# Kernel optimization log

Hardware: AMD Instinct MI355X
Metric: run time of the kernel (lower is better)

## Reference

```python
import jax, jax.numpy as jnp
import numpy as np

B, S, D, H = 4, 2048, 512, 8
DEPTH = D // H
EPS = 1e-6

def setup_inputs() -> dict:
    key = jax.random.key(0)
    ks = jax.random.split(key, 5)
    scale = 1.0 / np.sqrt(D)
    return {
        "x": jax.random.normal(ks[0], (B, S, D), dtype=jnp.float32),
        "wq": jax.random.normal(ks[1], (D, D), dtype=jnp.float32) * scale,
        "wk": jax.random.normal(ks[2], (D, D), dtype=jnp.float32) * scale,
        "wv": jax.random.normal(ks[3], (D, D), dtype=jnp.float32) * scale,
        "wo": jax.random.normal(ks[4], (D, D), dtype=jnp.float32) * scale,
        "bo": jnp.zeros((D,), dtype=jnp.float32),
        "gamma": jnp.ones((D,), dtype=jnp.float32),
        "beta": jnp.zeros((D,), dtype=jnp.float32),
    }

def _split_heads(t):
    # [B,S,D] -> [B,H,S,depth]
    return t.reshape(B, S, H, DEPTH).transpose(0, 2, 1, 3)

def reference(x, wq, wk, wv, wo, bo, gamma, beta):
    q = _split_heads(x @ wq)
    k = _split_heads(x @ wk)
    v = _split_heads(x @ wv)
    logits = jnp.einsum("bhqd,bhkd->bhqk", q, k) / jnp.sqrt(jnp.float32(DEPTH))
    attn = jax.nn.softmax(logits, axis=-1)  # dropout is identity at inference
    ctx = jnp.einsum("bhqk,bhkd->bhqd", attn, v)
    ctx = ctx.transpose(0, 2, 1, 3).reshape(B, S, D)
    out = ctx @ wo + bo
    resid = x + out  # output dropout identity at inference
    mu = jnp.mean(resid, axis=-1, keepdims=True)
    var = jnp.mean(jnp.square(resid - mu), axis=-1, keepdims=True)
    return (resid - mu) / jnp.sqrt(var + EPS) * gamma + beta
```

## Files before the change

kernel.cpp:

```cpp
#include <hip/hip_runtime.h>
#include <hip/hip_bf16.h>

typedef __attribute__((ext_vector_type(8))) short short8;
typedef __attribute__((ext_vector_type(4))) float f32x4;

constexpr int B_ = 4, S_ = 2048, D_ = 512, H_ = 8, DP_ = 64;
constexpr int M_ = B_ * S_;

__device__ __forceinline__ unsigned short f2b(float f) {
    __hip_bfloat16 h = __float2bfloat16(f);
    return *reinterpret_cast<unsigned short*>(&h);
}

__device__ __forceinline__ void gload_lds16(const unsigned short* g, unsigned short* l) {
    __builtin_amdgcn_global_load_lds((const __attribute__((address_space(1))) void*)g,
                                     (__attribute__((address_space(3))) void*)l, 16, 0, 0);
}

#define MFMA16(a, b, c) __builtin_amdgcn_mfma_f32_16x16x32_bf16((a), (b), (c), 0, 0, 0)
#define ASM_BAR() asm volatile("s_barrier" ::: "memory")

__global__ __launch_bounds__(256)
void convert_x(const float* __restrict__ in, unsigned short* __restrict__ out) {
    int i = blockIdx.x * 256 + threadIdx.x;
    float4 v = ((const float4*)in)[i];
    ushort4 o;
    o.x = f2b(v.x); o.y = f2b(v.y); o.z = f2b(v.z); o.w = f2b(v.w);
    ((ushort4*)out)[i] = o;
}

__global__ __launch_bounds__(256)
void transpose_w(const float* __restrict__ w0, const float* __restrict__ w1,
                 const float* __restrict__ w2, const float* __restrict__ w3,
                 unsigned short* __restrict__ outw) {
    const float* in = (blockIdx.z == 0) ? w0 : (blockIdx.z == 1) ? w1
                     : (blockIdx.z == 2) ? w2 : w3;
    unsigned short* out = outw + (size_t)blockIdx.z * D_ * D_;
    __shared__ float t[64][65];
    int k0 = blockIdx.x * 64, n0 = blockIdx.y * 64;
    int tx = threadIdx.x & 63, ty = threadIdx.x >> 6;
#pragma unroll
    for (int i = 0; i < 16; i++) {
        int r = ty * 16 + i;
        t[r][tx] = in[(size_t)(k0 + r) * D_ + n0 + tx];
    }
    __syncthreads();
#pragma unroll
    for (int i = 0; i < 16; i++) {
        int r = ty * 16 + i;
        out[(size_t)(n0 + r) * D_ + k0 + tx] = f2b(t[tx][r]);
    }
}

__global__ __launch_bounds__(256, 2)
void gemm_qkv(const unsigned short* __restrict__ X,
              const unsigned short* __restrict__ Wt,
              unsigned short* __restrict__ QKV) {
    const unsigned short* Bt = Wt + (size_t)blockIdx.z * D_ * D_;
    unsigned short* out = QKV + (size_t)blockIdx.z * M_ * D_;
    int m0 = blockIdx.x * 128, n0 = blockIdx.y * 128;
    int tid = threadIdx.x;
    int wave = tid >> 6, lane = tid & 63, l16 = lane & 15, quad = lane >> 4;
    int wm = (wave >> 1) * 64, wn = (wave & 1) * 64;

    __shared__ __align__(16) unsigned short As[128][40];
    __shared__ __align__(16) unsigned short Bs[128][40];

    f32x4 acc[4][4];
    const f32x4 zf = {0.f, 0.f, 0.f, 0.f};
#pragma unroll
    for (int i = 0; i < 4; i++)
#pragma unroll
        for (int j = 0; j < 4; j++) acc[i][j] = zf;

    for (int k0 = 0; k0 < D_; k0 += 32) {
        __syncthreads();
#pragma unroll
        for (int i = 0; i < 2; i++) {
            int c = tid + i * 256;
            int row = c >> 2, off = (c & 3) * 8;
            *(short8*)&As[row][off] = *(const short8*)(X + (size_t)(m0 + row) * D_ + k0 + off);
            *(short8*)&Bs[row][off] = *(const short8*)(Bt + (size_t)(n0 + row) * D_ + k0 + off);
        }
        __syncthreads();
        short8 af[4], bf[4];
#pragma unroll
        for (int mt = 0; mt < 4; mt++) af[mt] = *(const short8*)&As[wm + mt * 16 + l16][quad * 8];
#pragma unroll
        for (int nt = 0; nt < 4; nt++) bf[nt] = *(const short8*)&Bs[wn + nt * 16 + l16][quad * 8];
#pragma unroll
        for (int mt = 0; mt < 4; mt++)
#pragma unroll
            for (int nt = 0; nt < 4; nt++)
                acc[mt][nt] = MFMA16(af[mt], bf[nt], acc[mt][nt]);
    }
#pragma unroll
    for (int mt = 0; mt < 4; mt++)
#pragma unroll
        for (int nt = 0; nt < 4; nt++)
#pragma unroll
            for (int r = 0; r < 4; r++) {
                int m = m0 + wm + mt * 16 + quad * 4 + r;
                int n = n0 + wn + nt * 16 + l16;
                int bb = m >> 11, ss = m & 2047, hh = n >> 6, dd = n & 63;
                out[(((size_t)bb * H_ + hh) * S_ + ss) * DP_ + dd] = f2b(acc[mt][nt][r]);
            }
}

__global__ __launch_bounds__(256, 2)
void gemm_vt(const unsigned short* __restrict__ X,
             const unsigned short* __restrict__ Wt,
             unsigned short* __restrict__ Vt) {
    int bb = blockIdx.z;
    int m0 = blockIdx.x * 128, n0 = blockIdx.y * 128;
    int tid = threadIdx.x;
    int wave = tid >> 6, lane = tid & 63, l16 = lane & 15, quad = lane >> 4;
    int wm = (wave >> 1) * 64, wn = (wave & 1) * 64;

    __shared__ __align__(16) unsigned short As[128][40];
    __shared__ __align__(16) unsigned short Bs[128][40];

    f32x4 acc[4][4];
    const f32x4 zf = {0.f, 0.f, 0.f, 0.f};
#pragma unroll
    for (int i = 0; i < 4; i++)
#pragma unroll
        for (int j = 0; j < 4; j++) acc[i][j] = zf;

    for (int k0 = 0; k0 < D_; k0 += 32) {
        __syncthreads();
#pragma unroll
        for (int i = 0; i < 2; i++) {
            int c = tid + i * 256;
            int row = c >> 2, off = (c & 3) * 8;
            *(short8*)&As[row][off] = *(const short8*)(Wt + (size_t)(m0 + row) * D_ + k0 + off);
            *(short8*)&Bs[row][off] = *(const short8*)(X + (size_t)(bb * S_ + n0 + row) * D_ + k0 + off);
        }
        __syncthreads();
        short8 af[4], bf[4];
#pragma unroll
        for (int mt = 0; mt < 4; mt++) af[mt] = *(const short8*)&As[wm + mt * 16 + l16][quad * 8];
#pragma unroll
        for (int nt = 0; nt < 4; nt++) bf[nt] = *(const short8*)&Bs[wn + nt * 16 + l16][quad * 8];
#pragma unroll
        for (int mt = 0; mt < 4; mt++)
#pragma unroll
            for (int nt = 0; nt < 4; nt++)
                acc[mt][nt] = MFMA16(af[mt], bf[nt], acc[mt][nt]);
    }
#pragma unroll
    for (int mt = 0; mt < 4; mt++)
#pragma unroll
        for (int nt = 0; nt < 4; nt++)
#pragma unroll
            for (int r = 0; r < 4; r++) {
                int m = m0 + wm + mt * 16 + quad * 4 + r;
                int n = n0 + wn + nt * 16 + l16;
                Vt[((size_t)bb * D_ + m) * S_ + n] = f2b(acc[mt][nt][r]);
            }
}

__global__ __launch_bounds__(256, 4)
void flash_attn(const unsigned short* __restrict__ Qg, const unsigned short* __restrict__ Kg,
                const unsigned short* __restrict__ Vt, unsigned short* __restrict__ ctx) {
    int bid0 = blockIdx.x;
    int bid = (bid0 & 7) * 128 + (bid0 >> 3);
    int qt = bid & 31, hh = (bid >> 5) & 7, bb = bid >> 8;
    int tid = threadIdx.x;
    int wave = tid >> 6, lane = tid & 63, l16 = lane & 15, quad = lane >> 4;
    int qh = quad >> 1, ql = quad & 1;

    size_t bh = ((size_t)bb * H_ + hh) * S_ * DP_;
    const unsigned short* Qb = Qg + bh;
    const unsigned short* Kb = Kg + bh;
    const unsigned short* Vb = Vt + bh;

    __shared__ __align__(16) unsigned short Kls[2][64][64];
    __shared__ __align__(16) unsigned short Vls[2][64][64];
    __shared__ __align__(16) unsigned short Ps[4][16][64];

    const int psw = l16 & 7;
    const int drow = (lane >> 3) & 7;
    const int dsw = (lane & 7) ^ drow;

    short8 qf0, qf1;
    {
        const unsigned short* qp = Qb + (size_t)(qt * 64 + wave * 16 + l16) * DP_ + quad * 8;
        qf0 = *(const short8*)qp;
        qf1 = *(const short8*)(qp + 32);
    }

    auto stage = [&](int kv, int b) {
#pragma unroll
        for (int j = 0; j < 2; j++) {
            int r8 = (wave * 2 + j) * 8;
            int r = r8 + drow;
            gload_lds16(Kb + (size_t)(kv + r) * DP_ + dsw * 8, &Kls[b][r8][0]);
            gload_lds16(Vb + (size_t)r * S_ + kv + dsw * 8,    &Vls[b][r8][0]);
        }
    };

    stage(0, 0);
    stage(64, 1);
    asm volatile("s_waitcnt vmcnt(4)" ::: "memory");
    ASM_BAR();

    const f32x4 zf = {0.f, 0.f, 0.f, 0.f};
    f32x4 oacc[4];
#pragma unroll
    for (int i = 0; i < 4; i++) oacc[i] = zf;
    float m2 = -1e30f;
    float lrow = 0.f;
    constexpr float c1 = 0.125f * 1.44269504088896f;

    int cur = 0;
    for (int t = 0; t < 32; t++) {
        __builtin_amdgcn_s_setprio(1);
        f32x4 sacc[4];
#pragma unroll
        for (int nt = 0; nt < 4; nt++) {
            const unsigned short* kr = &Kls[cur][nt * 16 + l16][0];
            short8 kf0 = *(const short8*)(kr + ((quad ^ psw) * 8));
            short8 kf1 = *(const short8*)(kr + (((quad ^ 4) ^ psw) * 8));
            f32x4 s = zf;
            s = MFMA16(kf0, qf0, s);
            s = MFMA16(kf1, qf1, s);
            sacc[nt] = s;
        }
        __builtin_amdgcn_s_setprio(0);

        float t4[4];
#pragma unroll
        for (int nt = 0; nt < 4; nt++)
            t4[nt] = fmaxf(fmaxf(sacc[nt][0], sacc[nt][1]), fmaxf(sacc[nt][2], sacc[nt][3]));
        float g = fmaxf(fmaxf(t4[0], t4[1]), fmaxf(t4[2], t4[3]));
        g = fmaxf(g, __shfl_xor(g, 16));
        g = fmaxf(g, __shfl_xor(g, 32));
        g *= c1;
        float alpha = 1.0f;
        bool need = !__all(g <= m2 + 8.0f);
        if (need) {
            float m2n = fmaxf(m2, g);
            alpha = __builtin_amdgcn_exp2f(m2 - m2n);
            m2 = m2n;
        }
        float rs = 0.f;
#pragma unroll
        for (int nt = 0; nt < 4; nt++) {
            float p0 = __builtin_amdgcn_exp2f(__builtin_fmaf(sacc[nt][0], c1, -m2));
            float p1 = __builtin_amdgcn_exp2f(__builtin_fmaf(sacc[nt][1], c1, -m2));
            float p2 = __builtin_amdgcn_exp2f(__builtin_fmaf(sacc[nt][2], c1, -m2));
            float p3 = __builtin_amdgcn_exp2f(__builtin_fmaf(sacc[nt][3], c1, -m2));
            rs += (p0 + p1) + (p2 + p3);
            ushort4 pk;
            pk.x = f2b(p0); pk.y = f2b(p1); pk.z = f2b(p2); pk.w = f2b(p3);
            int c8 = (2 * nt + qh) ^ psw;
            *(ushort4*)&Ps[wave][l16][c8 * 8 + 4 * ql] = pk;
        }
        rs += __shfl_xor(rs, 16);
        rs += __shfl_xor(rs, 32);
        lrow = alpha * lrow + rs;
        if (need) {
            float al0 = __shfl(alpha, quad * 4 + 0);
            float al1 = __shfl(alpha, quad * 4 + 1);
            float al2 = __shfl(alpha, quad * 4 + 2);
            float al3 = __shfl(alpha, quad * 4 + 3);
#pragma unroll
            for (int ot = 0; ot < 4; ot++) {
                oacc[ot][0] *= al0; oacc[ot][1] *= al1;
                oacc[ot][2] *= al2; oacc[ot][3] *= al3;
            }
        }

        __builtin_amdgcn_s_setprio(1);
#pragma unroll
        for (int kt = 0; kt < 2; kt++) {
            int pc = ((kt * 4 + quad) ^ psw) * 8;
            short8 pf = *(const short8*)&Ps[wave][l16][pc];
#pragma unroll
            for (int ot = 0; ot < 4; ot++) {
                short8 vf = *(const short8*)&Vls[cur][ot * 16 + l16][pc];
                oacc[ot] = MFMA16(pf, vf, oacc[ot]);
            }
        }
        __builtin_amdgcn_s_setprio(0);

        ASM_BAR();
        if (t < 30) {
            stage((t + 2) * 64, cur);
            asm volatile("s_waitcnt vmcnt(4)" ::: "memory");
        } else {
            asm volatile("s_waitcnt vmcnt(0)" ::: "memory");
        }
        ASM_BAR();
        cur ^= 1;
    }

    float lb0 = __shfl(lrow, quad * 4 + 0);
    float lb1 = __shfl(lrow, quad * 4 + 1);
    float lb2 = __shfl(lrow, quad * 4 + 2);
    float lb3 = __shfl(lrow, quad * 4 + 3);
    float iv0 = __builtin_amdgcn_rcpf(lb0);
    float iv1 = __builtin_amdgcn_rcpf(lb1);
    float iv2 = __builtin_amdgcn_rcpf(lb2);
    float iv3 = __builtin_amdgcn_rcpf(lb3);
#pragma unroll
    for (int ot = 0; ot < 4; ot++) {
        int srow0 = qt * 64 + wave * 16 + quad * 4;
        size_t base = ((size_t)bb * S_ + srow0) * D_ + hh * DP_ + ot * 16 + l16;
        ctx[base]          = f2b(oacc[ot][0] * iv0);
        ctx[base + D_]     = f2b(oacc[ot][1] * iv1);
        ctx[base + 2 * D_] = f2b(oacc[ot][2] * iv2);
        ctx[base + 3 * D_] = f2b(oacc[ot][3] * iv3);
    }
}

__global__ __launch_bounds__(256, 2)
void gemm_proj(const unsigned short* __restrict__ A,
               const unsigned short* __restrict__ Bt,
               float* __restrict__ outf) {
    int m0 = blockIdx.x * 128, n0 = blockIdx.y * 128;
    int tid = threadIdx.x;
    int wave = tid >> 6, lane = tid & 63, l16 = lane & 15, quad = lane >> 4;
    int wm = (wave >> 1) * 64, wn = (wave & 1) * 64;

    __shared__ __align__(16) unsigned short As[128][40];
    __shared__ __align__(16) unsigned short Bs[128][40];

    f32x4 acc[4][4];
    const f32x4 zf = {0.f, 0.f, 0.f, 0.f};
#pragma unroll
    for (int i = 0; i < 4; i++)
#pragma unroll
        for (int j = 0; j < 4; j++) acc[i][j] = zf;

    for (int k0 = 0; k0 < D_; k0 += 32) {
        __syncthreads();
#pragma unroll
        for (int i = 0; i < 2; i++) {
            int c = tid + i * 256;
            int row = c >> 2, off = (c & 3) * 8;
            *(short8*)&As[row][off] = *(const short8*)(A + (size_t)(m0 + row) * D_ + k0 + off);
            *(short8*)&Bs[row][off] = *(const short8*)(Bt + (size_t)(n0 + row) * D_ + k0 + off);
        }
        __syncthreads();
        short8 af[4], bf[4];
#pragma unroll
        for (int mt = 0; mt < 4; mt++) af[mt] = *(const short8*)&As[wm + mt * 16 + l16][quad * 8];
#pragma unroll
        for (int nt = 0; nt < 4; nt++) bf[nt] = *(const short8*)&Bs[wn + nt * 16 + l16][quad * 8];
#pragma unroll
        for (int mt = 0; mt < 4; mt++)
#pragma unroll
            for (int nt = 0; nt < 4; nt++)
                acc[mt][nt] = MFMA16(af[mt], bf[nt], acc[mt][nt]);
    }
#pragma unroll
    for (int mt = 0; mt < 4; mt++)
#pragma unroll
        for (int nt = 0; nt < 4; nt++)
#pragma unroll
            for (int r = 0; r < 4; r++) {
                int m = m0 + wm + mt * 16 + quad * 4 + r;
                int n = n0 + wn + nt * 16 + l16;
                outf[(size_t)m * D_ + n] = acc[mt][nt][r];
            }
}

__global__ __launch_bounds__(256, 4)
void ln_out(const float* __restrict__ tmp, const float* __restrict__ Xg,
            const float* __restrict__ bo, const float* __restrict__ gamma,
            const float* __restrict__ beta, float* __restrict__ outp) {
    int row = blockIdx.x;
    int tid = threadIdx.x;
    int lane = tid & 63, wave = tid >> 6;
    float resid[2];
#pragma unroll
    for (int i = 0; i < 2; i++) {
        int c = tid + i * 256;
        resid[i] = Xg[(size_t)row * D_ + c] + tmp[(size_t)row * D_ + c] + bo[c];
    }
    float sum = resid[0] + resid[1];
    float sq = resid[0] * resid[0] + resid[1] * resid[1];
#pragma unroll
    for (int off = 1; off < 64; off <<= 1) {
        sum += __shfl_xor(sum, off);
        sq += __shfl_xor(sq, off);
    }
    __shared__ float red[8];
    if (lane == 0) { red[wave] = sum; red[4 + wave] = sq; }
    __syncthreads();
    sum = red[0] + red[1] + red[2] + red[3];
    sq = red[4] + red[5] + red[6] + red[7];
    float mu = sum * (1.0f / D_);
    float var = sq * (1.0f / D_) - mu * mu;
    float rstd = rsqrtf(var + 1e-6f);
#pragma unroll
    for (int i = 0; i < 2; i++) {
        int c = tid + i * 256;
        float o = (resid[i] - mu) * rstd * gamma[c] + beta[c];
        outp[(size_t)row * D_ + c] = o;
    }
}

extern "C" void kernel_launch(void* const* d_in, const int* in_sizes, int n_in,
                              void* d_out, int out_size, void* d_ws, size_t ws_size,
                              hipStream_t stream) {
    const float* x     = (const float*)d_in[0];
    const float* wq    = (const float*)d_in[1];
    const float* wk    = (const float*)d_in[2];
    const float* wv    = (const float*)d_in[3];
    const float* wo    = (const float*)d_in[4];
    const float* bo    = (const float*)d_in[5];
    const float* gamma = (const float*)d_in[6];
    const float* beta  = (const float*)d_in[7];
    float* out = (float*)d_out;

    unsigned short* xb  = (unsigned short*)d_ws;
    unsigned short* wt  = xb + (size_t)M_ * D_;
    unsigned short* Q   = wt + 4 * D_ * D_;
    unsigned short* K   = Q + (size_t)M_ * D_;
    unsigned short* Vt  = K + (size_t)M_ * D_;
    unsigned short* ctx = xb;
    float* tmp = (float*)Q;

    convert_x<<<dim3(M_ * D_ / 4 / 256), 256, 0, stream>>>(x, xb);
    transpose_w<<<dim3(8, 8, 4), 256, 0, stream>>>(wq, wk, wv, wo, wt);
    gemm_qkv<<<dim3(64, 4, 2), 256, 0, stream>>>(xb, wt, Q);
    gemm_vt<<<dim3(4, 16, 4), 256, 0, stream>>>(xb, wt + 2 * (size_t)D_ * D_, Vt);
    flash_attn<<<dim3(1024), 256, 0, stream>>>(Q, K, Vt, ctx);
    gemm_proj<<<dim3(64, 4), 256, 0, stream>>>(ctx, wt + 3 * (size_t)D_ * D_, tmp);
    ln_out<<<dim3(8192), 256, 0, stream>>>(tmp, x, bo, gamma, beta, out);
}
```

Before: 199.8 us.

## Use direct global-to-LDS loads with XOR swizzle in GEMMs and wave-per-row layernorm

The three GEMM kernels now stage 64-wide K tiles with global_load_lds straight into XOR-swizzled shared memory, replacing register-staged copies. This halves the number of barrier pairs per K loop, and the launch bounds are raised to 3 blocks per CU. LayerNorm now maps one wave to each row with float4 loads, which removes the shared-memory reduction and its barrier. Risks include more LDS use per block and register pressure under the tighter launch bounds.

```diff
diff --git a/kernel.cpp b/kernel.cpp
--- a/kernel.cpp
+++ b/kernel.cpp
@@ -52,7 +52,8 @@
     }
 }
 
-__global__ __launch_bounds__(256, 2)
+
+__global__ __launch_bounds__(256, 3)
 void gemm_qkv(const unsigned short* __restrict__ X,
               const unsigned short* __restrict__ Wt,
               unsigned short* __restrict__ QKV) {
@@ -63,8 +64,12 @@
     int wave = tid >> 6, lane = tid & 63, l16 = lane & 15, quad = lane >> 4;
     int wm = (wave >> 1) * 64, wn = (wave & 1) * 64;
 
-    __shared__ __align__(16) unsigned short As[128][40];
-    __shared__ __align__(16) unsigned short Bs[128][40];
+    __shared__ __align__(16) unsigned short As[128][64];
+    __shared__ __align__(16) unsigned short Bs[128][64];
+
+    const int psw = l16 & 7;
+    const int drow = lane >> 3;
+    const int dsw = (lane & 7) ^ drow;
 
     f32x4 acc[4][4];
     const f32x4 zf = {0.f, 0.f, 0.f, 0.f};
@@ -73,26 +78,30 @@
 #pragma unroll
         for (int j = 0; j < 4; j++) acc[i][j] = zf;
 
-    for (int k0 = 0; k0 < D_; k0 += 32) {
-        __syncthreads();
-#pragma unroll
-        for (int i = 0; i < 2; i++) {
-            int c = tid + i * 256;
-            int row = c >> 2, off = (c & 3) * 8;
-            *(short8*)&As[row][off] = *(const short8*)(X + (size_t)(m0 + row) * D_ + k0 + off);
-            *(short8*)&Bs[row][off] = *(const short8*)(Bt + (size_t)(n0 + row) * D_ + k0 + off);
-        }
-        __syncthreads();
-        short8 af[4], bf[4];
-#pragma unroll
-        for (int mt = 0; mt < 4; mt++) af[mt] = *(const short8*)&As[wm + mt * 16 + l16][quad * 8];
-#pragma unroll
-        for (int nt = 0; nt < 4; nt++) bf[nt] = *(const short8*)&Bs[wn + nt * 16 + l16][quad * 8];
-#pragma unroll
-        for (int mt = 0; mt < 4; mt++)
+    for (int k0 = 0; k0 < D_; k0 += 64) {
+        __syncthreads();
+#pragma unroll
+        for (int j = 0; j < 4; j++) {
+            int r8 = wave * 32 + j * 8;
+            gload_lds16(X  + (size_t)(m0 + r8 + drow) * D_ + k0 + dsw * 8, &As[r8][0]);
+            gload_lds16(Bt + (size_t)(n0 + r8 + drow) * D_ + k0 + dsw * 8, &Bs[r8][0]);
+        }
+        __syncthreads();
+#pragma unroll
+        for (int h = 0; h < 2; h++) {
+            short8 af[4], bf[4];
+#pragma unroll
+            for (int mt = 0; mt < 4; mt++)
+                af[mt] = *(const short8*)&As[wm + mt * 16 + l16][((h * 4 + quad) ^ psw) * 8];
 #pragma unroll
             for (int nt = 0; nt < 4; nt++)
-                acc[mt][nt] = MFMA16(af[mt], bf[nt], acc[mt][nt]);
+                bf[nt] = *(const short8*)&Bs[wn + nt * 16 + l16][((h * 4 + quad) ^ psw) * 8];
+#pragma unroll
+            for (int mt = 0; mt < 4; mt++)
+#pragma unroll
+                for (int nt = 0; nt < 4; nt++)
+                    acc[mt][nt] = MFMA16(af[mt], bf[nt], acc[mt][nt]);
+        }
     }
 #pragma unroll
     for (int mt = 0; mt < 4; mt++)
@@ -107,7 +116,7 @@
             }
 }
 
-__global__ __launch_bounds__(256, 2)
+__global__ __launch_bounds__(256, 3)
 void gemm_vt(const unsigned short* __restrict__ X,
              const unsigned short* __restrict__ Wt,
              unsigned short* __restrict__ Vt) {
@@ -117,8 +126,12 @@
     int wave = tid >> 6, lane = tid & 63, l16 = lane & 15, quad = lane >> 4;
     int wm = (wave >> 1) * 64, wn = (wave & 1) * 64;
 
-    __shared__ __align__(16) unsigned short As[128][40];
-    __shared__ __align__(16) unsigned short Bs[128][40];
+    __shared__ __align__(16) unsigned short As[128][64];
+    __shared__ __align__(16) unsigned short Bs[128][64];
+
+    const int psw = l16 & 7;
+    const int drow = lane >> 3;
+    const int dsw = (lane & 7) ^ drow;
 
     f32x4 acc[4][4];
     const f32x4 zf = {0.f, 0.f, 0.f, 0.f};
@@ -127,26 +140,30 @@
 #pragma unroll
         for (int j = 0; j < 4; j++) acc[i][j] = zf;
 
-    for (int k0 = 0; k0 < D_; k0 += 32) {
-        __syncthreads();
-#pragma unroll
-        for (int i = 0; i < 2; i++) {
-            int c = tid + i * 256;
-            int row = c >> 2, off = (c & 3) * 8;
-            *(short8*)&As[row][off] = *(const short8*)(Wt + (size_t)(m0 + row) * D_ + k0 + off);
-            *(short8*)&Bs[row][off] = *(const short8*)(X + (size_t)(bb * S_ + n0 + row) * D_ + k0 + off);
-        }
-        __syncthreads();
-        short8 af[4], bf[4];
-#pragma unroll
-        for (int mt = 0; mt < 4; mt++) af[mt] = *(const short8*)&As[wm + mt * 16 + l16][quad * 8];
-#pragma unroll
-        for (int nt = 0; nt < 4; nt++) bf[nt] = *(const short8*)&Bs[wn + nt * 16 + l16][quad * 8];
-#pragma unroll
-        for (int mt = 0; mt < 4; mt++)
+    for (int k0 = 0; k0 < D_; k0 += 64) {
+        __syncthreads();
+#pragma unroll
+        for (int j = 0; j < 4; j++) {
+            int r8 = wave * 32 + j * 8;
+            gload_lds16(Wt + (size_t)(m0 + r8 + drow) * D_ + k0 + dsw * 8,            &As[r8][0]);
+            gload_lds16(X  + (size_t)(bb * S_ + n0 + r8 + drow) * D_ + k0 + dsw * 8,  &Bs[r8][0]);
+        }
+        __syncthreads();
+#pragma unroll
+        for (int h = 0; h < 2; h++) {
+            short8 af[4], bf[4];
+#pragma unroll
+            for (int mt = 0; mt < 4; mt++)
+                af[mt] = *(const short8*)&As[wm + mt * 16 + l16][((h * 4 + quad) ^ psw) * 8];
 #pragma unroll
             for (int nt = 0; nt < 4; nt++)
-                acc[mt][nt] = MFMA16(af[mt], bf[nt], acc[mt][nt]);
+                bf[nt] = *(const short8*)&Bs[wn + nt * 16 + l16][((h * 4 + quad) ^ psw) * 8];
+#pragma unroll
+            for (int mt = 0; mt < 4; mt++)
+#pragma unroll
+                for (int nt = 0; nt < 4; nt++)
+                    acc[mt][nt] = MFMA16(af[mt], bf[nt], acc[mt][nt]);
+        }
     }
 #pragma unroll
     for (int mt = 0; mt < 4; mt++)
@@ -315,7 +332,7 @@
     }
 }
 
-__global__ __launch_bounds__(256, 2)
+__global__ __launch_bounds__(256, 3)
 void gemm_proj(const unsigned short* __restrict__ A,
                const unsigned short* __restrict__ Bt,
                float* __restrict__ outf) {
@@ -324,8 +341,12 @@
     int wave = tid >> 6, lane = tid & 63, l16 = lane & 15, quad = lane >> 4;
     int wm = (wave >> 1) * 64, wn = (wave & 1) * 64;
 
-    __shared__ __align__(16) unsigned short As[128][40];
-    __shared__ __align__(16) unsigned short Bs[128][40];
+    __shared__ __align__(16) unsigned short As[128][64];
+    __shared__ __align__(16) unsigned short Bs[128][64];
+
+    const int psw = l16 & 7;
+    const int drow = lane >> 3;
+    const int dsw = (lane & 7) ^ drow;
 
     f32x4 acc[4][4];
     const f32x4 zf = {0.f, 0.f, 0.f, 0.f};
@@ -334,26 +355,30 @@
 #pragma unroll
         for (int j = 0; j < 4; j++) acc[i][j] = zf;
 
-    for (int k0 = 0; k0 < D_; k0 += 32) {
-        __syncthreads();
-#pragma unroll
-        for (int i = 0; i < 2; i++) {
-            int c = tid + i * 256;
-            int row = c >> 2, off = (c & 3) * 8;
-            *(short8*)&As[row][off] = *(const short8*)(A + (size_t)(m0 + row) * D_ + k0 + off);
-            *(short8*)&Bs[row][off] = *(const short8*)(Bt + (size_t)(n0 + row) * D_ + k0 + off);
-        }
-        __syncthreads();
-        short8 af[4], bf[4];
-#pragma unroll
-        for (int mt = 0; mt < 4; mt++) af[mt] = *(const short8*)&As[wm + mt * 16 + l16][quad * 8];
-#pragma unroll
-        for (int nt = 0; nt < 4; nt++) bf[nt] = *(const short8*)&Bs[wn + nt * 16 + l16][quad * 8];
-#pragma unroll
-        for (int mt = 0; mt < 4; mt++)
+    for (int k0 = 0; k0 < D_; k0 += 64) {
+        __syncthreads();
+#pragma unroll
+        for (int j = 0; j < 4; j++) {
+            int r8 = wave * 32 + j * 8;
+            gload_lds16(A  + (size_t)(m0 + r8 + drow) * D_ + k0 + dsw * 8, &As[r8][0]);
+            gload_lds16(Bt + (size_t)(n0 + r8 + drow) * D_ + k0 + dsw * 8, &Bs[r8][0]);
+        }
+        __syncthreads();
+#pragma unroll
+        for (int h = 0; h < 2; h++) {
+            short8 af[4], bf[4];
+#pragma unroll
+            for (int mt = 0; mt < 4; mt++)
+                af[mt] = *(const short8*)&As[wm + mt * 16 + l16][((h * 4 + quad) ^ psw) * 8];
 #pragma unroll
             for (int nt = 0; nt < 4; nt++)
-                acc[mt][nt] = MFMA16(af[mt], bf[nt], acc[mt][nt]);
+                bf[nt] = *(const short8*)&Bs[wn + nt * 16 + l16][((h * 4 + quad) ^ psw) * 8];
+#pragma unroll
+            for (int mt = 0; mt < 4; mt++)
+#pragma unroll
+                for (int nt = 0; nt < 4; nt++)
+                    acc[mt][nt] = MFMA16(af[mt], bf[nt], acc[mt][nt]);
+        }
     }
 #pragma unroll
     for (int mt = 0; mt < 4; mt++)
@@ -367,39 +392,50 @@
             }
 }
 
-__global__ __launch_bounds__(256, 4)
+__global__ __launch_bounds__(256, 8)
 void ln_out(const float* __restrict__ tmp, const float* __restrict__ Xg,
             const float* __restrict__ bo, const float* __restrict__ gamma,
             const float* __restrict__ beta, float* __restrict__ outp) {
-    int row = blockIdx.x;
-    int tid = threadIdx.x;
-    int lane = tid & 63, wave = tid >> 6;
-    float resid[2];
+    int wave = threadIdx.x >> 6, lane = threadIdx.x & 63;
+    int row = blockIdx.x * 4 + wave;
+    const float4* t4 = (const float4*)(tmp + (size_t)row * D_);
+    const float4* x4 = (const float4*)(Xg + (size_t)row * D_);
+    const float4* b4 = (const float4*)bo;
+    const float4* g4 = (const float4*)gamma;
+    const float4* e4 = (const float4*)beta;
+    float4* o4 = (float4*)(outp + (size_t)row * D_);
+
+    float4 r[2];
+    float sum = 0.f, sq = 0.f;
 #pragma unroll
     for (int i = 0; i < 2; i++) {
-        int c = tid + i * 256;
-        resid[i] = Xg[(size_t)row * D_ + c] + tmp[(size_t)row * D_ + c] + bo[c];
-    }
-    float sum = resid[0] + resid[1];
-    float sq = resid[0] * resid[0] + resid[1] * resid[1];
+        int c = lane + i * 64;
+        float4 a = t4[c], x = x4[c], b = b4[c];
+        r[i].x = a.x + x.x + b.x;
+        r[i].y = a.y + x.y + b.y;
+        r[i].z = a.z + x.z + b.z;
+        r[i].w = a.w + x.w + b.w;
+        sum += (r[i].x + r[i].y) + (r[i].z + r[i].w);
+        sq += (r[i].x * r[i].x + r[i].y * r[i].y) + (r[i].z * r[i].z + r[i].w * r[i].w);
+    }
 #pragma unroll
     for (int off = 1; off < 64; off <<= 1) {
         sum += __shfl_xor(sum, off);
         sq += __shfl_xor(sq, off);
     }
-    __shared__ float red[8];
-    if (lane == 0) { red[wave] = sum; red[4 + wave] = sq; }
-    __syncthreads();
-    sum = red[0] + red[1] + red[2] + red[3];
-    sq = red[4] + red[5] + red[6] + red[7];
     float mu = sum * (1.0f / D_);
     float var = sq * (1.0f / D_) - mu * mu;
     float rstd = rsqrtf(var + 1e-6f);
 #pragma unroll
     for (int i = 0; i < 2; i++) {
-        int c = tid + i * 256;
-        float o = (resid[i] - mu) * rstd * gamma[c] + beta[c];
-        outp[(size_t)row * D_ + c] = o;
+        int c = lane + i * 64;
+        float4 g = g4[c], e = e4[c];
+        float4 o;
+        o.x = (r[i].x - mu) * rstd * g.x + e.x;
+        o.y = (r[i].y - mu) * rstd * g.y + e.y;
+        o.z = (r[i].z - mu) * rstd * g.z + e.z;
+        o.w = (r[i].w - mu) * rstd * g.w + e.w;
+        o4[c] = o;
     }
 }
 
@@ -430,5 +466,5 @@
     gemm_vt<<<dim3(4, 16, 4), 256, 0, stream>>>(xb, wt + 2 * (size_t)D_ * D_, Vt);
     flash_attn<<<dim3(1024), 256, 0, stream>>>(Q, K, Vt, ctx);
     gemm_proj<<<dim3(64, 4), 256, 0, stream>>>(ctx, wt + 3 * (size_t)D_ * D_, tmp);
-    ln_out<<<dim3(8192), 256, 0, stream>>>(tmp, x, bo, gamma, beta, out);
-}
+    ln_out<<<dim3(2048), 256, 0, stream>>>(tmp, x, bo, gamma, beta, out);
+}
```

After: 188.4 us. 5.7% less time.
